# Performance work log

Measured on AMD Instinct MI355X. Metric: run time of the kernel, lower is better.

The kernel has to match this reference:

```python
import jax, jax.numpy as jnp
import numpy as np

D_MODEL = 1024
NUM_HEADS = 16
DEPTH = D_MODEL // NUM_HEADS
MAX_LEN = 5000


def _make_pe(d_model=D_MODEL, max_len=MAX_LEN):
    # Faithful to torch PositionalEncoding: pe shape [max_len, 1, d_model]
    position = np.arange(max_len, dtype=np.float32)[:, None]
    div_term = np.exp(np.arange(0, d_model, 2, dtype=np.float32) * (-np.log(10000.0) / d_model))
    pe = np.zeros((max_len, d_model), dtype=np.float32)
    pe[:, 0::2] = np.sin(position * div_term)
    pe[:, 1::2] = np.cos(position * div_term)
    return jnp.asarray(pe[:, None, :])  # [max_len, 1, d_model]


def setup_inputs() -> dict:
    key = jax.random.key(0)
    ks = jax.random.split(key, 11)
    B, S, D = 4, 2048, D_MODEL
    s = 1.0 / np.sqrt(D)
    inp = {
        "v": jax.random.normal(ks[0], (B, S, D), jnp.float32),
        "k": jax.random.normal(ks[1], (B, S, D), jnp.float32),
        "q": jax.random.normal(ks[2], (B, S, D), jnp.float32),
        "wq_w": jax.random.normal(ks[3], (D, D), jnp.float32) * s,
        "wq_b": jnp.zeros((D,), jnp.float32),
        "wk_w": jax.random.normal(ks[4], (D, D), jnp.float32) * s,
        "wk_b": jnp.zeros((D,), jnp.float32),
        "wv_w": jax.random.normal(ks[5], (D, D), jnp.float32) * s,
        "wv_b": jnp.zeros((D,), jnp.float32),
        "dense_w": jax.random.normal(ks[6], (D, D), jnp.float32) * s,
        "dense_b": jnp.zeros((D,), jnp.float32),
        "pe": _make_pe(),
    }
    return inp


def _split_heads(x, B):
    # [B, S, D] -> [B, H, S, depth]
    return x.reshape(B, -1, NUM_HEADS, DEPTH).transpose(0, 2, 1, 3)


def reference(v, k, q, wq_w, wq_b, wk_w, wk_b, wv_w, wv_b, dense_w, dense_b, pe):
    B = q.shape[0]
    # Faithful bug-reproduction: pe[:batch] has shape [B, 1, D], broadcast over seq.
    pe_b = pe[:B]  # [B, 1, D]
    q = q + pe_b
    k = k + pe_b
    v = v + pe_b
    # Linear layers (torch: x @ W.T + b)
    qh = _split_heads(q @ wq_w.T + wq_b, B)  # [B,H,Sq,d]
    kh = _split_heads(k @ wk_w.T + wk_b, B)  # [B,H,Sk,d]
    vh = _split_heads(v @ wv_w.T + wv_b, B)  # [B,H,Sk,d]
    scale = 1.0 / jnp.sqrt(jnp.float32(DEPTH))
    logits = jnp.einsum("bhqd,bhkd->bhqk", qh, kh) * scale
    attn = jax.nn.softmax(logits, axis=-1)
    out = jnp.einsum("bhqk,bhkd->bhqd", attn, vh)
    out = out.transpose(0, 2, 1, 3).reshape(B, -1, D_MODEL)
    return out @ dense_w.T + dense_b
```

## Files before the change

### kernel.cpp

```cpp
#include <hip/hip_runtime.h>
#include <hip/hip_bf16.h>

typedef short short8 __attribute__((ext_vector_type(8)));
typedef float f32x16 __attribute__((ext_vector_type(16)));
typedef unsigned int uint4v __attribute__((ext_vector_type(4)));

#define MFMA32(a, b, c) __builtin_amdgcn_mfma_f32_32x32x16_bf16(a, b, c, 0, 0, 0)

typedef __attribute__((address_space(1))) const unsigned int gas_u32;
typedef __attribute__((address_space(3))) unsigned int las_u32;

__device__ inline void gll16(const void* g, void* l) {
    __builtin_amdgcn_global_load_lds((gas_u32*)g, (las_u32*)l, 16, 0, 0);
}

__device__ inline unsigned short f2bf(float f) {
    unsigned u = __builtin_bit_cast(unsigned, f);
    u += 0x7fff + ((u >> 16) & 1);
    return (unsigned short)(u >> 16);
}

__device__ inline unsigned pk_trunc(float a, float b) {
    unsigned ua = __builtin_bit_cast(unsigned, a);
    unsigned ub = __builtin_bit_cast(unsigned, b);
    return (ua >> 16) | (ub & 0xFFFF0000u);
}

__device__ inline float exp2_fast(float x) {
#if __has_builtin(__builtin_amdgcn_exp2f)
    return __builtin_amdgcn_exp2f(x);
#else
    float r; asm("v_exp_f32 %0, %1" : "=v"(r) : "v"(x)); return r;
#endif
}

__device__ inline void pl32_swap(unsigned &a, unsigned &b) {
    asm volatile("v_permlane32_swap_b32 %0, %1" : "+v"(a), "+v"(b));
}

__global__ void pe_cast3(const float* __restrict__ q, const float* __restrict__ k,
                         const float* __restrict__ v, const float* __restrict__ pe,
                         unsigned short* __restrict__ oq, unsigned short* __restrict__ ok,
                         unsigned short* __restrict__ ov) {
    const float* x = (blockIdx.y == 0) ? q : (blockIdx.y == 1) ? k : v;
    unsigned short* o = (blockIdx.y == 0) ? oq : (blockIdx.y == 1) ? ok : ov;
    int i = blockIdx.x * 256 + threadIdx.x;
    long e = (long)i * 4;
    int b = (int)(e >> 21);
    int d = (int)(e & 1023);
    float4 xv = reinterpret_cast<const float4*>(x)[i];
    float4 pv = *reinterpret_cast<const float4*>(pe + b * 1024 + d);
    ushort4 r;
    r.x = f2bf(xv.x + pv.x); r.y = f2bf(xv.y + pv.y);
    r.z = f2bf(xv.z + pv.z); r.w = f2bf(xv.w + pv.w);
    reinterpret_cast<ushort4*>(o)[i] = r;
}

__global__ void wcast4(const float* __restrict__ w0, const float* __restrict__ w1,
                       const float* __restrict__ w2, const float* __restrict__ w3,
                       unsigned short* __restrict__ o0) {
    const float* w = (blockIdx.y == 0) ? w0 : (blockIdx.y == 1) ? w1
                   : (blockIdx.y == 2) ? w2 : w3;
    unsigned short* o = o0 + (size_t)blockIdx.y * 1024 * 1024;
    int i = blockIdx.x * 256 + threadIdx.x;
    float4 xv = reinterpret_cast<const float4*>(w)[i];
    ushort4 r;
    r.x = f2bf(xv.x); r.y = f2bf(xv.y); r.z = f2bf(xv.z); r.w = f2bf(xv.w);
    reinterpret_cast<ushort4*>(o)[i] = r;
}

template <int BM, int MF, int MODE>
__global__ __launch_bounds__(512, 2) void gemm2(const unsigned short* __restrict__ A0,
                                                const unsigned short* __restrict__ W0,
                                                const float* __restrict__ bq,
                                                const float* __restrict__ bk,
                                                const float* __restrict__ bv,
                                                void* __restrict__ oq,
                                                void* __restrict__ ok,
                                                void* __restrict__ ov,
                                                float qscale) {
    const int NT = 16;
    constexpr int AR = BM / 64;
    __shared__ __align__(16) unsigned short lsA[2][BM * 64];
    __shared__ __align__(16) unsigned short lsB[2][256 * 64];

    int z = (MODE == 3) ? blockIdx.z : 0;
    const unsigned short* A = A0 + (size_t)z * 8192 * 1024;
    const unsigned short* W = W0 + (size_t)z * 1024 * 1024;
    const float* bias = (MODE == 3) ? ((z == 0) ? bq : (z == 1) ? bk : bv) : bq;
    float scale = (MODE == 3 && z == 0) ? qscale : 1.0f;

    int tid = threadIdx.x, wave = tid >> 6, lane = tid & 63;
    int l31 = lane & 31, hi = lane >> 5;
    int wr = wave >> 2, wc = wave & 3;
    int brow = blockIdx.x * BM;
    int bcol = blockIdx.y * 256;

    int rowt = tid >> 3;
    int colsw = (tid & 7) * 8 ^ ((rowt & 7) << 3);
    const unsigned short* srcA = A + (long)(brow + rowt) * 1024 + colsw;
    const unsigned short* srcB = W + (long)(bcol + rowt) * 1024 + colsw;

    f32x16 acc[MF][2];
#pragma unroll
    for (int mf = 0; mf < MF; ++mf)
#pragma unroll
        for (int nf = 0; nf < 2; ++nf)
#pragma unroll
            for (int r = 0; r < 16; ++r) acc[mf][nf][r] = 0.f;

#define STG(t, bi) do {                                                       \
        _Pragma("unroll")                                                     \
        for (int rr = 0; rr < AR; ++rr)                                       \
            gll16(srcA + (t) * 64 + rr * 65536,                               \
                  (char*)lsA[bi] + (rr * 512 + wave * 64) * 16);              \
        _Pragma("unroll")                                                     \
        for (int rr = 0; rr < 4; ++rr)                                        \
            gll16(srcB + (t) * 64 + rr * 65536,                               \
                  (char*)lsB[bi] + (rr * 512 + wave * 64) * 16);              \
    } while (0)

    STG(0, 0);
    __syncthreads();

    int cur = 0;
    for (int t = 0; t < NT; ++t) {
        if (t < NT - 1) STG(t + 1, cur ^ 1);

        const char* KA = (const char*)lsA[cur];
        const char* KB = (const char*)lsB[cur];
#pragma unroll
        for (int ks = 0; ks < 4; ++ks) {
            int cofs = (ks * 32 + hi * 16) ^ ((l31 & 7) << 4);
            short8 af[MF], bf[2];
#pragma unroll
            for (int mf = 0; mf < MF; ++mf)
                af[mf] = *(const short8*)(KA + (wr * (MF * 32) + mf * 32 + l31) * 128 + cofs);
#pragma unroll
            for (int nf = 0; nf < 2; ++nf)
                bf[nf] = *(const short8*)(KB + (wc * 64 + nf * 32 + l31) * 128 + cofs);
#pragma unroll
            for (int mf = 0; mf < MF; ++mf)
#pragma unroll
                for (int nf = 0; nf < 2; ++nf)
                    acc[mf][nf] = MFMA32(af[mf], bf[nf], acc[mf][nf]);
        }
        __syncthreads();
        cur ^= 1;
    }
#undef STG

    void* out = (MODE == 3) ? ((z == 0) ? oq : (z == 1) ? ok : ov) : oq;
#pragma unroll
    for (int mf = 0; mf < MF; ++mf)
#pragma unroll
        for (int nf = 0; nf < 2; ++nf) {
            int col = bcol + wc * 64 + nf * 32 + l31;
            float bv_ = bias[col];
#pragma unroll
            for (int r = 0; r < 16; ++r) {
                int row = brow + wr * (MF * 32) + mf * 32 + (r & 3) + 8 * (r >> 2) + 4 * hi;
                float v = (acc[mf][nf][r] + bv_) * scale;
                if (MODE == 1) {
                    ((float*)out)[(long)row * 1024 + col] = v;
                } else {
                    int b = row >> 11, s = row & 2047;
                    if (z < 2) {
                        int h = col >> 6, d = col & 63;
                        ((unsigned short*)out)[(((long)(b * 16 + h) * 2048 + s) * 64 + d)] = f2bf(v);
                    } else {
                        ((unsigned short*)out)[((long)(b * 1024 + col)) * 2048 + s] = f2bf(v);
                    }
                }
            }
        }
}

__global__ __launch_bounds__(256, 2) void attn_kernel(const unsigned short* __restrict__ Qh,
                                                      const unsigned short* __restrict__ Kh,
                                                      const unsigned short* __restrict__ Vt,
                                                      unsigned short* __restrict__ Om) {
    const int S = 2048;
    const int NT = S / 64;
    int flat = blockIdx.x;
    int nf_ = (flat & 7) * 64 + (flat >> 3);
    int qt = nf_ & 7;
    int bh = nf_ >> 3;
    int b = bh >> 4, h = bh & 15;

    int tid = threadIdx.x, wave = tid >> 6, lane = tid & 63;
    int l31 = lane & 31, hi = lane >> 5;

    __shared__ __align__(16) unsigned short Kl[3][4096];
    __shared__ __align__(16) unsigned short Vtl[3][4096];

    const unsigned short* Qb = Qh + (long)bh * S * 64;
    const unsigned short* Kb = Kh + (long)bh * S * 64;
    const unsigned short* Vb = Vt + (long)bh * 64 * S;

    int colS = ((((tid & 7) * 16) ^ (((tid >> 3) & 7) << 4)) >> 1);
    const unsigned short* srcK = Kb + (tid >> 3) * 64 + colS;
    const unsigned short* srcV = Vb + (tid >> 3) * 2048 + colS;

    short8 aq[2][4];
    {
        const unsigned short* qrow = Qb + (long)(qt * 256 + wave * 64 + l31) * 64 + hi * 8;
#pragma unroll
        for (int qf = 0; qf < 2; ++qf)
#pragma unroll
            for (int s = 0; s < 4; ++s)
                aq[qf][s] = *(const short8*)(qrow + qf * 32 * 64 + s * 16);
    }

    f32x16 oacc[2][2], lacc[2];
#pragma unroll
    for (int r = 0; r < 16; ++r) {
        oacc[0][0][r] = 0.f; oacc[0][1][r] = 0.f;
        oacc[1][0][r] = 0.f; oacc[1][1][r] = 0.f;
        lacc[0][r] = 0.f; lacc[1][r] = 0.f;
    }

    const short8 ones8 = {0x3F80, 0x3F80, 0x3F80, 0x3F80, 0x3F80, 0x3F80, 0x3F80, 0x3F80};

    int rb0 = l31 * 128;
    int swz = (l31 & 7) << 4;

#define STAGE(kt, bi) do {                                              \
        const unsigned short* sk = srcK + (kt) * 4096;                  \
        gll16(sk,         (char*)Kl[bi] + wave * 1024);                 \
        gll16(sk + 2048,  (char*)Kl[bi] + 4096 + wave * 1024);          \
        const unsigned short* sv = srcV + (kt) * 64;                    \
        gll16(sv,         (char*)Vtl[bi] + wave * 1024);                \
        gll16(sv + 65536, (char*)Vtl[bi] + 4096 + wave * 1024);         \
    } while (0)

    STAGE(0, 0);
    STAGE(1, 1);

    int bi = 0, sb = 2;
    for (int kt = 0; kt < NT; ++kt) {
        if (kt == NT - 1) { asm volatile("s_waitcnt vmcnt(0)" ::: "memory"); }
        else              { asm volatile("s_waitcnt vmcnt(4)" ::: "memory"); }
        __builtin_amdgcn_s_barrier();
        if (kt < NT - 2) STAGE(kt + 2, sb);

        const char* KlC = (const char*)Kl[bi];
        const char* VlC = (const char*)Vtl[bi];

        f32x16 sacc[2][2];
#pragma unroll
        for (int r = 0; r < 16; ++r) {
            sacc[0][0][r] = 0.f; sacc[0][1][r] = 0.f;
            sacc[1][0][r] = 0.f; sacc[1][1][r] = 0.f;
        }
#pragma unroll
        for (int blk = 0; blk < 2; ++blk)
#pragma unroll
            for (int s = 0; s < 4; ++s) {
                short8 kf = *(const short8*)(KlC + blk * 4096 + rb0 + ((32 * s + 16 * hi) ^ swz));
                sacc[0][blk] = MFMA32(kf, aq[0][s], sacc[0][blk]);
                sacc[1][blk] = MFMA32(kf, aq[1][s], sacc[1][blk]);
            }

#pragma unroll
        for (int qf = 0; qf < 2; ++qf)
#pragma unroll
            for (int blk = 0; blk < 2; ++blk)
#pragma unroll
                for (int r = 0; r < 16; ++r) sacc[qf][blk][r] = exp2_fast(sacc[qf][blk][r]);

#pragma unroll
        for (int s = 0; s < 4; ++s) {
            const int blk = s >> 1, base = (s & 1) * 8;
            short8 pa[2];
#pragma unroll
            for (int qf = 0; qf < 2; ++qf) {
                unsigned q0 = pk_trunc(sacc[qf][blk][base + 0], sacc[qf][blk][base + 1]);
                unsigned q1 = pk_trunc(sacc[qf][blk][base + 2], sacc[qf][blk][base + 3]);
                unsigned q2 = pk_trunc(sacc[qf][blk][base + 4], sacc[qf][blk][base + 5]);
                unsigned q3 = pk_trunc(sacc[qf][blk][base + 6], sacc[qf][blk][base + 7]);
                pl32_swap(q0, q2);
                pl32_swap(q1, q3);
                uint4v pw; pw[0] = q0; pw[1] = q1; pw[2] = q2; pw[3] = q3;
                pa[qf] = __builtin_bit_cast(short8, pw);
            }
#pragma unroll
            for (int dblk = 0; dblk < 2; ++dblk) {
                short8 vf = *(const short8*)(VlC + dblk * 4096 + rb0 + ((32 * s + 16 * hi) ^ swz));
                oacc[0][dblk] = MFMA32(pa[0], vf, oacc[0][dblk]);
                oacc[1][dblk] = MFMA32(pa[1], vf, oacc[1][dblk]);
            }
            lacc[0] = MFMA32(pa[0], ones8, lacc[0]);
            lacc[1] = MFMA32(pa[1], ones8, lacc[1]);
        }
        bi = (bi == 2) ? 0 : bi + 1;
        sb = (sb == 2) ? 0 : sb + 1;
    }
#undef STAGE

#pragma unroll
    for (int qf = 0; qf < 2; ++qf) {
        float inv[16];
#pragma unroll
        for (int r = 0; r < 16; ++r) inv[r] = 1.0f / lacc[qf][r];
        int qrow0 = qt * 256 + wave * 64 + qf * 32 + 4 * hi;
#pragma unroll
        for (int dblk = 0; dblk < 2; ++dblk)
#pragma unroll
            for (int r = 0; r < 16; ++r) {
                int qrow = qrow0 + (r & 3) + 8 * (r >> 2);
                int d = h * 64 + dblk * 32 + l31;
                float v = oacc[qf][dblk][r] * inv[r];
                Om[((long)b * 2048 + qrow) * 1024 + d] = f2bf(v);
            }
    }
}

extern "C" void kernel_launch(void* const* d_in, const int* in_sizes, int n_in,
                              void* d_out, int out_size, void* d_ws, size_t ws_size,
                              hipStream_t stream) {
    const float* v_in = (const float*)d_in[0];
    const float* k_in = (const float*)d_in[1];
    const float* q_in = (const float*)d_in[2];
    const float* wq_w = (const float*)d_in[3];
    const float* wq_b = (const float*)d_in[4];
    const float* wk_w = (const float*)d_in[5];
    const float* wk_b = (const float*)d_in[6];
    const float* wv_w = (const float*)d_in[7];
    const float* wv_b = (const float*)d_in[8];
    const float* wd_w = (const float*)d_in[9];
    const float* wd_b = (const float*)d_in[10];
    const float* pe   = (const float*)d_in[11];

    const long SZ = 8192L * 1024 * 2;
    char* ws = (char*)d_ws;
    unsigned short* xq = (unsigned short*)(ws + 0);
    unsigned short* xk = (unsigned short*)(ws + SZ);
    unsigned short* xv = (unsigned short*)(ws + 2 * SZ);
    unsigned short* qh = (unsigned short*)(ws + 3 * SZ);
    unsigned short* kh = (unsigned short*)(ws + 4 * SZ);
    unsigned short* vt = (unsigned short*)(ws + 5 * SZ);
    unsigned short* wqb16 = (unsigned short*)(ws + 6 * SZ);

    pe_cast3<<<dim3(8192, 3), 256, 0, stream>>>(q_in, k_in, v_in, pe, xq, xk, xv);
    wcast4<<<dim3(1024, 4), 256, 0, stream>>>(wq_w, wk_w, wv_w, wd_w, wqb16);

    const float QSCALE = 0.125f * 1.44269504088896f;
    gemm2<256, 4, 3><<<dim3(32, 4, 3), 512, 0, stream>>>(
        xq, wqb16, wq_b, wk_b, wv_b, qh, kh, vt, QSCALE);

    unsigned short* om = xq;
    attn_kernel<<<512, 256, 0, stream>>>(qh, kh, vt, om);

    gemm2<128, 2, 1><<<dim3(64, 4, 1), 512, 0, stream>>>(
        om, wqb16 + 3L * 1024 * 1024, wd_b, nullptr, nullptr, d_out, nullptr, nullptr, 1.0f);
}
```

Baseline: 231.3 us.

## Rewrite projection GEMMs with 128x128 tiles and 16x16x32 MFMA

Replaces the 512-thread GEMM that used 256-wide tiles and 32x32 MFMA with a 256-thread kernel using 128x128 tiles, a K-step of 32 and 16x16x32 bf16 MFMA. It also drops the XOR swizzle in LDS and launches more, smaller blocks so more of them fit on each CU. The goal is better occupancy and CU coverage for the QKV and output projections. The cost is more K iterations with a barrier each, lower reuse per tile, and likely LDS bank conflicts from the unswizzled 64-byte row reads.

```diff
diff --git a/kernel.cpp b/kernel.cpp
--- a/kernel.cpp
+++ b/kernel.cpp
@@ -2,9 +2,11 @@
 #include <hip/hip_bf16.h>
 
 typedef short short8 __attribute__((ext_vector_type(8)));
+typedef float f32x4 __attribute__((ext_vector_type(4)));
 typedef float f32x16 __attribute__((ext_vector_type(16)));
 typedef unsigned int uint4v __attribute__((ext_vector_type(4)));
 
+#define MFMA16(a, b, c) __builtin_amdgcn_mfma_f32_16x16x32_bf16(a, b, c, 0, 0, 0)
 #define MFMA32(a, b, c) __builtin_amdgcn_mfma_f32_32x32x16_bf16(a, b, c, 0, 0, 0)
 
 typedef __attribute__((address_space(1))) const unsigned int gas_u32;
@@ -69,8 +71,8 @@
     reinterpret_cast<ushort4*>(o)[i] = r;
 }
 
-template <int BM, int MF, int MODE>
-__global__ __launch_bounds__(512, 2) void gemm2(const unsigned short* __restrict__ A0,
+template <int MODE>
+__global__ __launch_bounds__(256, 4) void gemm3(const unsigned short* __restrict__ A0,
                                                 const unsigned short* __restrict__ W0,
                                                 const float* __restrict__ bq,
                                                 const float* __restrict__ bk,
@@ -79,10 +81,9 @@
                                                 void* __restrict__ ok,
                                                 void* __restrict__ ov,
                                                 float qscale) {
-    const int NT = 16;
-    constexpr int AR = BM / 64;
-    __shared__ __align__(16) unsigned short lsA[2][BM * 64];
-    __shared__ __align__(16) unsigned short lsB[2][256 * 64];
+    const int NT = 32;
+    __shared__ unsigned short lsA[2][128 * 32];
+    __shared__ unsigned short lsB[2][128 * 32];
 
     int z = (MODE == 3) ? blockIdx.z : 0;
     const unsigned short* A = A0 + (size_t)z * 8192 * 1024;
@@ -90,34 +91,28 @@
     const float* bias = (MODE == 3) ? ((z == 0) ? bq : (z == 1) ? bk : bv) : bq;
     float scale = (MODE == 3 && z == 0) ? qscale : 1.0f;
 
-    int tid = threadIdx.x, wave = tid >> 6, lane = tid & 63;
-    int l31 = lane & 31, hi = lane >> 5;
-    int wr = wave >> 2, wc = wave & 3;
-    int brow = blockIdx.x * BM;
-    int bcol = blockIdx.y * 256;
-
-    int rowt = tid >> 3;
-    int colsw = (tid & 7) * 8 ^ ((rowt & 7) << 3);
-    const unsigned short* srcA = A + (long)(brow + rowt) * 1024 + colsw;
-    const unsigned short* srcB = W + (long)(bcol + rowt) * 1024 + colsw;
-
-    f32x16 acc[MF][2];
-#pragma unroll
-    for (int mf = 0; mf < MF; ++mf)
-#pragma unroll
-        for (int nf = 0; nf < 2; ++nf)
-#pragma unroll
-            for (int r = 0; r < 16; ++r) acc[mf][nf][r] = 0.f;
-
-#define STG(t, bi) do {                                                       \
-        _Pragma("unroll")                                                     \
-        for (int rr = 0; rr < AR; ++rr)                                       \
-            gll16(srcA + (t) * 64 + rr * 65536,                               \
-                  (char*)lsA[bi] + (rr * 512 + wave * 64) * 16);              \
-        _Pragma("unroll")                                                     \
-        for (int rr = 0; rr < 4; ++rr)                                        \
-            gll16(srcB + (t) * 64 + rr * 65536,                               \
-                  (char*)lsB[bi] + (rr * 512 + wave * 64) * 16);              \
+    int tid = threadIdx.x;
+    int wave = tid >> 6, lane = tid & 63, lg = lane >> 4, l15 = lane & 15;
+    int brow = blockIdx.x * 128;
+    int bcol = blockIdx.y * 128;
+    int wr = wave >> 1, wc = wave & 1;
+
+    f32x4 zero4 = {0.f, 0.f, 0.f, 0.f};
+    f32x4 acc[4][4];
+#pragma unroll
+    for (int m = 0; m < 4; ++m)
+#pragma unroll
+        for (int n = 0; n < 4; ++n) acc[m][n] = zero4;
+
+#define STG(k0, bi) do {                                                        \
+        _Pragma("unroll")                                                       \
+        for (int j = 0; j < 2; ++j) {                                           \
+            int c = j * 256 + wave * 64 + lane;                                 \
+            gll16(A + ((long)(brow + (c >> 2)) * 1024 + (k0) + (c & 3) * 8),    \
+                  (char*)lsA[bi] + (j * 256 + wave * 64) * 16);                 \
+            gll16(W + ((long)(bcol + (c >> 2)) * 1024 + (k0) + (c & 3) * 8),    \
+                  (char*)lsB[bi] + (j * 256 + wave * 64) * 16);                 \
+        }                                                                       \
     } while (0)
 
     STG(0, 0);
@@ -125,26 +120,26 @@
 
     int cur = 0;
     for (int t = 0; t < NT; ++t) {
-        if (t < NT - 1) STG(t + 1, cur ^ 1);
+        if (t < NT - 1) STG((t + 1) * 32, cur ^ 1);
 
         const char* KA = (const char*)lsA[cur];
         const char* KB = (const char*)lsB[cur];
-#pragma unroll
-        for (int ks = 0; ks < 4; ++ks) {
-            int cofs = (ks * 32 + hi * 16) ^ ((l31 & 7) << 4);
-            short8 af[MF], bf[2];
-#pragma unroll
-            for (int mf = 0; mf < MF; ++mf)
-                af[mf] = *(const short8*)(KA + (wr * (MF * 32) + mf * 32 + l31) * 128 + cofs);
-#pragma unroll
-            for (int nf = 0; nf < 2; ++nf)
-                bf[nf] = *(const short8*)(KB + (wc * 64 + nf * 32 + l31) * 128 + cofs);
-#pragma unroll
-            for (int mf = 0; mf < MF; ++mf)
-#pragma unroll
-                for (int nf = 0; nf < 2; ++nf)
-                    acc[mf][nf] = MFMA32(af[mf], bf[nf], acc[mf][nf]);
-        }
+        short8 af[4], bf_[4];
+#pragma unroll
+        for (int m = 0; m < 4; ++m) {
+            int row = wr * 64 + m * 16 + l15;
+            af[m] = *(const short8*)(KA + row * 64 + lg * 16);
+        }
+#pragma unroll
+        for (int n = 0; n < 4; ++n) {
+            int col = wc * 64 + n * 16 + l15;
+            bf_[n] = *(const short8*)(KB + col * 64 + lg * 16);
+        }
+#pragma unroll
+        for (int m = 0; m < 4; ++m)
+#pragma unroll
+            for (int n = 0; n < 4; ++n) acc[m][n] = MFMA16(af[m], bf_[n], acc[m][n]);
+
         __syncthreads();
         cur ^= 1;
     }
@@ -152,15 +147,15 @@
 
     void* out = (MODE == 3) ? ((z == 0) ? oq : (z == 1) ? ok : ov) : oq;
 #pragma unroll
-    for (int mf = 0; mf < MF; ++mf)
-#pragma unroll
-        for (int nf = 0; nf < 2; ++nf) {
-            int col = bcol + wc * 64 + nf * 32 + l31;
+    for (int m = 0; m < 4; ++m)
+#pragma unroll
+        for (int n = 0; n < 4; ++n) {
+            int col = bcol + wc * 64 + n * 16 + l15;
             float bv_ = bias[col];
 #pragma unroll
-            for (int r = 0; r < 16; ++r) {
-                int row = brow + wr * (MF * 32) + mf * 32 + (r & 3) + 8 * (r >> 2) + 4 * hi;
-                float v = (acc[mf][nf][r] + bv_) * scale;
+            for (int r = 0; r < 4; ++r) {
+                int row = brow + wr * 64 + m * 16 + lg * 4 + r;
+                float v = (acc[m][n][r] + bv_) * scale;
                 if (MODE == 1) {
                     ((float*)out)[(long)row * 1024 + col] = v;
                 } else {
@@ -346,12 +341,12 @@
     wcast4<<<dim3(1024, 4), 256, 0, stream>>>(wq_w, wk_w, wv_w, wd_w, wqb16);
 
     const float QSCALE = 0.125f * 1.44269504088896f;
-    gemm2<256, 4, 3><<<dim3(32, 4, 3), 512, 0, stream>>>(
+    gemm3<3><<<dim3(64, 8, 3), 256, 0, stream>>>(
         xq, wqb16, wq_b, wk_b, wv_b, qh, kh, vt, QSCALE);
 
     unsigned short* om = xq;
     attn_kernel<<<512, 256, 0, stream>>>(qh, kh, vt, om);
 
-    gemm2<128, 2, 1><<<dim3(64, 4, 1), 512, 0, stream>>>(
+    gemm3<1><<<dim3(64, 8, 1), 256, 0, stream>>>(
         om, wqb16 + 3L * 1024 * 1024, wd_b, nullptr, nullptr, d_out, nullptr, nullptr, 1.0f);
 }
```

Result: faster. 221.8 us (-4.1%).
